# Performance work log

Hardware: AMD Instinct MI355X
Metric: run time of the kernel (lower is better)

The kernel has to match this reference:

```python
import jax, jax.numpy as jnp
import numpy as np

B, L, D = 16, 1024, 256  # batch, c_len == q_len (required by the expand/add in the source), 2*d_model


def mask_logits(x, m):
    # Faithful to the source's (unusual) masking: x*m + x*(1-m)*1e30
    return x * m + x * (1.0 - m) * 1e30


def setup_inputs() -> dict:
    key = jax.random.key(0)
    k = jax.random.split(key, 7)
    c = jax.random.normal(k[0], (B, L, D), dtype=jnp.float32)
    q = jax.random.normal(k[1], (B, L, D), dtype=jnp.float32)
    c_mask = jnp.ones((B, 1, L), dtype=jnp.float32)
    q_mask = jnp.ones((B, 1, L), dtype=jnp.float32)
    # Learned parameters (nn.Parameter zeros in the source; random here so the test is non-degenerate)
    c_weight = jax.random.normal(k[2], (D, 1), dtype=jnp.float32) * 0.05
    q_weight = jax.random.normal(k[3], (D, 1), dtype=jnp.float32) * 0.05
    cq_weight = jax.random.normal(k[4], (1, 1, D), dtype=jnp.float32) * 0.05
    bias = jnp.zeros((1,), dtype=jnp.float32)
    return {"c": c, "q": q, "c_mask": c_mask, "q_mask": q_mask,
            "c_weight": c_weight, "q_weight": q_weight,
            "cq_weight": cq_weight, "bias": bias}


def reference(c, q, c_mask, q_mask, c_weight, q_weight, cq_weight, bias):
    # Dropout treated as identity (inference) for a deterministic reference.
    s0 = jnp.matmul(c, c_weight)                      # [B, L, 1] -> broadcasts over q_len
    s1 = jnp.swapaxes(jnp.matmul(c, q_weight), 1, 2)  # [B, 1, L] (source uses c here, not q)
    s2 = jnp.einsum('bid,bjd->bij', c * cq_weight, q) # [B, L, L]
    S = s0 + s1 + s2 + bias                           # trilinear similarity
    S1 = jax.nn.softmax(mask_logits(S, q_mask), axis=-1)              # [B, Lc, Lq]
    C2Q = jnp.matmul(S1, q)                                           # [B, Lc, D]
    # torch F.softmax with no dim on a 3D tensor defaults to dim=0 (legacy behavior) -> axis=0
    S2 = jax.nn.softmax(mask_logits(jnp.swapaxes(S, 1, 2), c_mask), axis=0)  # [B, Lq, Lc]
    S2 = jnp.matmul(S1, S2)                                           # [B, Lc, Lc]
    Q2C = jnp.matmul(S2, c)                                           # [B, Lc, D]
    # torch.cat default dim=0 -> [4B, Lc, D]
    return jnp.concatenate((c, C2Q, c * C2Q, c * Q2C), axis=0)
```

## Files before the change

### kernel.cpp

```cpp
#include <hip/hip_runtime.h>

typedef __bf16 bf16;
typedef _Float16 f16;
typedef __attribute__((ext_vector_type(8))) __bf16 bf16x8;
typedef __attribute__((ext_vector_type(4))) __bf16 bf16x4;
typedef __attribute__((ext_vector_type(8))) _Float16 f16x8;
typedef __attribute__((ext_vector_type(4))) _Float16 f16x4;
typedef __attribute__((ext_vector_type(4))) float f32x4;

constexpr int Bn = 16, Ln = 1024, Dn = 256;

__device__ __forceinline__ float maskf(float m) { return m + (1.0f - m) * 1e30f; }

__device__ __forceinline__ void gload16(const void* g, void* l) {
  __builtin_amdgcn_global_load_lds((const __attribute__((address_space(1))) void*)g,
                                   (__attribute__((address_space(3))) void*)l, 16, 0, 0);
}

#define VMCNT(N) asm volatile("s_waitcnt vmcnt(" #N ")" ::: "memory")
#define LGKM0 asm volatile("s_waitcnt lgkmcnt(0)" ::: "memory")
#define BARR                                  \
  do {                                        \
    asm volatile("" ::: "memory");            \
    __builtin_amdgcn_s_barrier();             \
    asm volatile("" ::: "memory");            \
  } while (0)

__device__ __forceinline__ void stage512(const bf16* __restrict__ G, int ldg, int k0,
                                         bf16* L, int tid, int wid) {
#pragma unroll
  for (int p = 0; p < 2; ++p) {
    int u = tid + (p << 9);
    int row = u >> 3, s = u & 7;
    int kk = ((s ^ (row & 7)) << 3);
    gload16(G + (size_t)row * ldg + k0 + kk, L + ((p << 9) + (wid << 6)) * 8);
  }
}

__device__ __forceinline__ const bf16* swzp(const bf16* L, int row, int slot) {
  return L + row * 64 + ((slot ^ (row & 7)) << 3);
}

__global__ __launch_bounds__(256) void k_prep2(
    const float* __restrict__ c, const float* __restrict__ q,
    const float* __restrict__ cw, const float* __restrict__ qw,
    const float* __restrict__ cqw, bf16* __restrict__ cm, bf16* __restrict__ qb,
    bf16* __restrict__ cT, bf16* __restrict__ qT,
    float* __restrict__ s0, float* __restrict__ s1, float* __restrict__ outc) {
  __shared__ __align__(16) bf16 tc[32][264];
  __shared__ __align__(16) bf16 tq[32][264];
  int blk = blockIdx.x;
  int b = blk >> 5;
  int l0 = (blk & 31) << 5;
  int t = threadIdx.x;
  int rl = t >> 3;
  int c0 = (t & 7) << 5;
  int grow = b * Ln + l0 + rl;
  size_t base = (size_t)grow * Dn + c0;
  float4 cv[8], qv[8];
#pragma unroll
  for (int k = 0; k < 8; ++k) {
    cv[k] = *(const float4*)&c[base + k * 4];
    qv[k] = *(const float4*)&q[base + k * 4];
  }
  float d0 = 0.f, d1 = 0.f;
#pragma unroll
  for (int k = 0; k < 8; ++k) {
    float4 w = *(const float4*)&cw[c0 + k * 4];
    float4 u = *(const float4*)&qw[c0 + k * 4];
    d0 += cv[k].x * w.x + cv[k].y * w.y + cv[k].z * w.z + cv[k].w * w.w;
    d1 += cv[k].x * u.x + cv[k].y * u.y + cv[k].z * u.z + cv[k].w * u.w;
  }
  d0 += __shfl_xor(d0, 1); d0 += __shfl_xor(d0, 2); d0 += __shfl_xor(d0, 4);
  d1 += __shfl_xor(d1, 1); d1 += __shfl_xor(d1, 2); d1 += __shfl_xor(d1, 4);
  if ((t & 7) == 0) { s0[grow] = d0; s1[grow] = d1; }
#pragma unroll
  for (int k = 0; k < 8; ++k) *(float4*)&outc[base + k * 4] = cv[k];
#pragma unroll
  for (int k2 = 0; k2 < 4; ++k2) {
    float4 m0 = *(const float4*)&cqw[c0 + k2 * 8];
    float4 m1 = *(const float4*)&cqw[c0 + k2 * 8 + 4];
    bf16x8 vm, vq, vc;
#pragma unroll
    for (int e = 0; e < 8; ++e) {
      float cvv = ((const float*)&cv[k2 * 2 + (e >> 2)])[e & 3];
      float qvv = ((const float*)&qv[k2 * 2 + (e >> 2)])[e & 3];
      float mw = (e < 4) ? ((const float*)&m0)[e] : ((const float*)&m1)[e - 4];
      vm[e] = (bf16)(cvv * mw);
      vq[e] = (bf16)qvv;
      vc[e] = (bf16)cvv;
    }
    *(bf16x8*)&cm[base + k2 * 8] = vm;
    *(bf16x8*)&qb[base + k2 * 8] = vq;
    *(bf16x8*)&tc[rl][c0 + k2 * 8] = vc;
    *(bf16x8*)&tq[rl][c0 + k2 * 8] = vq;
  }
  __syncthreads();
  int d = t;
  size_t tb = ((size_t)b * Dn + d) * Ln + l0;
  bf16x8 o[4];
#pragma unroll
  for (int j = 0; j < 4; ++j)
#pragma unroll
    for (int e = 0; e < 8; ++e) o[j][e] = tc[j * 8 + e][d];
#pragma unroll
  for (int j = 0; j < 4; ++j) *(bf16x8*)&cT[tb + j * 8] = o[j];
#pragma unroll
  for (int j = 0; j < 4; ++j)
#pragma unroll
    for (int e = 0; e < 8; ++e) o[j][e] = tq[j * 8 + e][d];
#pragma unroll
  for (int j = 0; j < 4; ++j) *(bf16x8*)&qT[tb + j * 8] = o[j];
}

__global__ __launch_bounds__(512) void g_s(const bf16* __restrict__ Am,
                                           const bf16* __restrict__ Bm,
                                           const float* __restrict__ s0,
                                           const float* __restrict__ s1,
                                           const float* __restrict__ bias,
                                           f16* __restrict__ S) {
  __shared__ __align__(16) bf16 lds[2][2 * 128 * 64];
  int f = blockIdx.x;
  int o = (f & 7) * 128 + (f >> 3);
  int bx = o & 7, by = (o >> 3) & 7, b = o >> 6;
  const bf16* Ab = Am + (size_t)b * Ln * Dn + (size_t)by * 128 * Dn;
  const bf16* Bb = Bm + (size_t)b * Ln * Dn + (size_t)bx * 128 * Dn;
  const int tid = threadIdx.x, wid = tid >> 6, lane = tid & 63;
  const int r = lane & 15, h = lane >> 4, wr = wid >> 2, wc = wid & 3;
  f32x4 acc[4][2];
  f32x4 zero = {0.f, 0.f, 0.f, 0.f};
#pragma unroll
  for (int i = 0; i < 4; ++i)
#pragma unroll
    for (int j = 0; j < 2; ++j) acc[i][j] = zero;

  stage512(Ab, Dn, 0, &lds[0][0], tid, wid);
  stage512(Bb, Dn, 0, &lds[0][8192], tid, wid);
  for (int t = 0; t < 4; ++t) {
    int cur = t & 1;
    if (t < 3) {
      stage512(Ab, Dn, (t + 1) * 64, &lds[cur ^ 1][0], tid, wid);
      stage512(Bb, Dn, (t + 1) * 64, &lds[cur ^ 1][8192], tid, wid);
      VMCNT(4);
    } else {
      VMCNT(0);
    }
    BARR;
    const bf16* lA = &lds[cur][0];
    const bf16* lB = &lds[cur][8192];
#pragma unroll
    for (int kk2 = 0; kk2 < 2; ++kk2) {
      int slot = (kk2 << 2) | h;
      bf16x8 av[4], bv[2];
#pragma unroll
      for (int i = 0; i < 4; ++i)
        av[i] = *(const bf16x8*)swzp(lA, (wr << 6) + (i << 4) + r, slot);
#pragma unroll
      for (int j = 0; j < 2; ++j)
        bv[j] = *(const bf16x8*)swzp(lB, (wc << 5) + (j << 4) + r, slot);
#pragma unroll
      for (int i = 0; i < 4; ++i)
#pragma unroll
        for (int j = 0; j < 2; ++j)
          acc[i][j] = __builtin_amdgcn_mfma_f32_16x16x32_bf16(av[i], bv[j], acc[i][j], 0, 0, 0);
    }
    LGKM0; BARR;
  }
  int grow = by * 128 + wr * 64, gcol = bx * 128 + wc * 32;
  float bvv = bias[0];
  size_t sb = (size_t)b * Ln * Ln;
#pragma unroll
  for (int j = 0; j < 2; ++j) {
    int n = gcol + j * 16 + r;
    float v1 = s1[b * Ln + n];
#pragma unroll
    for (int i = 0; i < 4; ++i) {
      int mb = grow + i * 16 + h * 4;
#pragma unroll
      for (int g = 0; g < 4; ++g) {
        float v0 = s0[b * Ln + mb + g];
        S[sb + (size_t)(mb + g) * Ln + n] = (f16)(acc[i][j][g] + v0 + v1 + bvv);
      }
    }
  }
}

__global__ __launch_bounds__(256) void k_sm(const f16* __restrict__ S,
                                            const float* __restrict__ qmask,
                                            const float* __restrict__ cmask,
                                            bf16* __restrict__ P1,
                                            bf16* __restrict__ P2) {
  __shared__ __align__(16) bf16 tile[16][32][36];
  int blk = blockIdx.x;
  int t = threadIdx.x;
  if (blk < 1024) {
    int i0 = (blk >> 5) << 5, j0 = (blk & 31) << 5;
    int ti = t >> 3, tj4 = (t & 7) << 2;
    int i = i0 + ti;
    const f16* Sp = S + (size_t)i * Ln + j0 + tj4;
    float fm[16];
#pragma unroll
    for (int b = 0; b < 16; ++b) fm[b] = maskf(cmask[b * Ln + i]);
    f16x4 u[16];
#pragma unroll
    for (int b = 0; b < 16; ++b) u[b] = *(const f16x4*)(Sp + (size_t)b * Ln * Ln);
    float m[4] = {-3.4e38f, -3.4e38f, -3.4e38f, -3.4e38f};
#pragma unroll
    for (int b = 0; b < 16; ++b)
#pragma unroll
      for (int g = 0; g < 4; ++g) m[g] = fmaxf(m[g], (float)u[b][g] * fm[b]);
    float e[16][4];
    float s[4] = {0.f, 0.f, 0.f, 0.f};
#pragma unroll
    for (int b = 0; b < 16; ++b)
#pragma unroll
      for (int g = 0; g < 4; ++g) {
        e[b][g] = __expf((float)u[b][g] * fm[b] - m[g]);
        s[g] += e[b][g];
      }
#pragma unroll
    for (int g = 0; g < 4; ++g) s[g] = 1.0f / s[g];
#pragma unroll
    for (int b = 0; b < 16; ++b)
#pragma unroll
      for (int g = 0; g < 4; ++g) tile[b][tj4 + g][ti] = (bf16)(e[b][g] * s[g]);
    __syncthreads();
    int jl = t >> 3, i4 = (t & 7) << 2;
#pragma unroll
    for (int b = 0; b < 16; ++b) {
      *(bf16x4*)&P2[((size_t)b * Ln + j0 + jl) * Ln + i0 + i4] =
          *(const bf16x4*)&tile[b][jl][i4];
    }
  } else {
    int row = (blk - 1024) * 4 + (t >> 6);
    int b = row >> 10;
    int lane = t & 63;
    const f16* Sr = S + (size_t)row * Ln;
    const float* qm = qmask + (size_t)b * Ln;
    float v[16];
    float mx = -3.4e38f;
#pragma unroll
    for (int p = 0; p < 2; ++p) {
      f16x8 x = ((const f16x8*)Sr)[lane + (p << 6)];
      float4 m0 = ((const float4*)qm)[(lane + (p << 6)) * 2];
      float4 m1 = ((const float4*)qm)[(lane + (p << 6)) * 2 + 1];
      float mm[8] = {m0.x, m0.y, m0.z, m0.w, m1.x, m1.y, m1.z, m1.w};
#pragma unroll
      for (int e = 0; e < 8; ++e) {
        float xv = (float)x[e] * maskf(mm[e]);
        v[8 * p + e] = xv;
        mx = fmaxf(mx, xv);
      }
    }
#pragma unroll
    for (int off = 32; off; off >>= 1) mx = fmaxf(mx, __shfl_xor(mx, off));
    float sum = 0.f;
#pragma unroll
    for (int k = 0; k < 16; ++k) {
      v[k] = __expf(v[k] - mx);
      sum += v[k];
    }
#pragma unroll
    for (int off = 32; off; off >>= 1) sum += __shfl_xor(sum, off);
    float inv = 1.0f / sum;
    bf16* Pr = P1 + (size_t)row * Ln;
#pragma unroll
    for (int p = 0; p < 2; ++p) {
      bf16x8 o;
#pragma unroll
      for (int e = 0; e < 8; ++e) o[e] = (bf16)(v[8 * p + e] * inv);
      ((bf16x8*)Pr)[lane + (p << 6)] = o;
    }
  }
}

__global__ __launch_bounds__(512) void g_t(const bf16* __restrict__ cT,
                                           const bf16* __restrict__ P2,
                                           bf16* __restrict__ TT) {
  __shared__ __align__(16) bf16 lds[2][2 * 128 * 64];
  int f = blockIdx.x;
  int o = (f & 7) * 32 + (f >> 3);
  int b = o >> 4, md = (o >> 3) & 1, nb = o & 7;
  const bf16* Ab = cT + (size_t)b * Dn * Ln + (size_t)md * 128 * Ln;
  const bf16* Bb = P2 + (size_t)b * Ln * Ln + (size_t)nb * 128 * Ln;
  const int tid = threadIdx.x, wid = tid >> 6, lane = tid & 63;
  const int r = lane & 15, h = lane >> 4, wr = wid >> 2, wc = wid & 3;
  f32x4 acc[4][2];
  f32x4 zero = {0.f, 0.f, 0.f, 0.f};
#pragma unroll
  for (int i = 0; i < 4; ++i)
#pragma unroll
    for (int j = 0; j < 2; ++j) acc[i][j] = zero;

  stage512(Ab, Ln, 0, &lds[0][0], tid, wid);
  stage512(Bb, Ln, 0, &lds[0][8192], tid, wid);
  for (int t = 0; t < 16; ++t) {
    int cur = t & 1;
    if (t < 15) {
      stage512(Ab, Ln, (t + 1) * 64, &lds[cur ^ 1][0], tid, wid);
      stage512(Bb, Ln, (t + 1) * 64, &lds[cur ^ 1][8192], tid, wid);
      VMCNT(4);
    } else {
      VMCNT(0);
    }
    BARR;
    const bf16* lA = &lds[cur][0];
    const bf16* lB = &lds[cur][8192];
#pragma unroll
    for (int kk2 = 0; kk2 < 2; ++kk2) {
      int slot = (kk2 << 2) | h;
      bf16x8 av[4], bv[2];
#pragma unroll
      for (int i = 0; i < 4; ++i)
        av[i] = *(const bf16x8*)swzp(lA, (wr << 6) + (i << 4) + r, slot);
#pragma unroll
      for (int j = 0; j < 2; ++j)
        bv[j] = *(const bf16x8*)swzp(lB, (wc << 5) + (j << 4) + r, slot);
#pragma unroll
      for (int i = 0; i < 4; ++i)
#pragma unroll
        for (int j = 0; j < 2; ++j)
          acc[i][j] = __builtin_amdgcn_mfma_f32_16x16x32_bf16(av[i], bv[j], acc[i][j], 0, 0, 0);
    }
    LGKM0; BARR;
  }
  size_t ob = (size_t)b * Dn * Ln;
  int dbase = md * 128 + wr * 64, cbase = nb * 128 + wc * 32;
#pragma unroll
  for (int i = 0; i < 4; ++i)
#pragma unroll
    for (int j = 0; j < 2; ++j) {
      int n = cbase + j * 16 + r;
#pragma unroll
      for (int g = 0; g < 4; ++g)
        TT[ob + (size_t)(dbase + i * 16 + h * 4 + g) * Ln + n] = (bf16)acc[i][j][g];
    }
}

__global__ __launch_bounds__(512) void g_cq(const bf16* __restrict__ P1,
                                            const bf16* __restrict__ qT,
                                            const bf16* __restrict__ TT,
                                            const float* __restrict__ c,
                                            float* __restrict__ out) {
  __shared__ __align__(16) bf16 lds[2][3 * 128 * 64];
  int f = blockIdx.x;
  int o = (f & 7) * 32 + (f >> 3);
  int b = o >> 4, by = (o >> 1) & 7, bx = o & 1;
  const bf16* Ab = P1 + (size_t)b * Ln * Ln + (size_t)by * 128 * Ln;
  const bf16* B1 = qT + (size_t)b * Dn * Ln + (size_t)bx * 128 * Ln;
  const bf16* B2 = TT + (size_t)b * Dn * Ln + (size_t)bx * 128 * Ln;
  const int tid = threadIdx.x, wid = tid >> 6, lane = tid & 63;
  const int r = lane & 15, h = lane >> 4, wr = wid >> 2, wc = wid & 3;
  f32x4 acc1[4][2], acc2[4][2];
  f32x4 zero = {0.f, 0.f, 0.f, 0.f};
#pragma unroll
  for (int i = 0; i < 4; ++i)
#pragma unroll
    for (int j = 0; j < 2; ++j) { acc1[i][j] = zero; acc2[i][j] = zero; }

  stage512(Ab, Ln, 0, &lds[0][0], tid, wid);
  stage512(B1, Ln, 0, &lds[0][8192], tid, wid);
  stage512(B2, Ln, 0, &lds[0][16384], tid, wid);
  for (int t = 0; t < 16; ++t) {
    int cur = t & 1;
    if (t < 15) {
      stage512(Ab, Ln, (t + 1) * 64, &lds[cur ^ 1][0], tid, wid);
      stage512(B1, Ln, (t + 1) * 64, &lds[cur ^ 1][8192], tid, wid);
      stage512(B2, Ln, (t + 1) * 64, &lds[cur ^ 1][16384], tid, wid);
      VMCNT(6);
    } else {
      VMCNT(0);
    }
    BARR;
    const bf16* lA = &lds[cur][0];
    const bf16* lB1 = &lds[cur][8192];
    const bf16* lB2 = &lds[cur][16384];
#pragma unroll
    for (int kk2 = 0; kk2 < 2; ++kk2) {
      int slot = (kk2 << 2) | h;
      bf16x8 av[4], bv[2];
#pragma unroll
      for (int i = 0; i < 4; ++i)
        av[i] = *(const bf16x8*)swzp(lA, (wr << 6) + (i << 4) + r, slot);
#pragma unroll
      for (int j = 0; j < 2; ++j)
        bv[j] = *(const bf16x8*)swzp(lB1, (wc << 5) + (j << 4) + r, slot);
#pragma unroll
      for (int i = 0; i < 4; ++i)
#pragma unroll
        for (int j = 0; j < 2; ++j)
          acc1[i][j] = __builtin_amdgcn_mfma_f32_16x16x32_bf16(av[i], bv[j], acc1[i][j], 0, 0, 0);
#pragma unroll
      for (int j = 0; j < 2; ++j)
        bv[j] = *(const bf16x8*)swzp(lB2, (wc << 5) + (j << 4) + r, slot);
#pragma unroll
      for (int i = 0; i < 4; ++i)
#pragma unroll
        for (int j = 0; j < 2; ++j)
          acc2[i][j] = __builtin_amdgcn_mfma_f32_16x16x32_bf16(av[i], bv[j], acc2[i][j], 0, 0, 0);
    }
    LGKM0; BARR;
  }

  int grow = by * 128 + wr * 64, gcol = bx * 128 + wc * 32;
  const float* cb = c + (size_t)b * Ln * Dn;
  float* o1 = out + (size_t)(1 * Bn + b) * Ln * Dn;
  float* o2 = out + (size_t)(2 * Bn + b) * Ln * Dn;
  float* o3 = out + (size_t)(3 * Bn + b) * Ln * Dn;
#pragma unroll
  for (int j = 0; j < 2; ++j) {
    int n = gcol + j * 16 + r;
#pragma unroll
    for (int i = 0; i < 4; ++i) {
      int mb = grow + i * 16 + h * 4;
#pragma unroll
      for (int g = 0; g < 4; ++g) {
        float v1 = acc1[i][j][g];
        float v2 = acc2[i][j][g];
        size_t off = (size_t)(mb + g) * Dn + n;
        float cc = cb[off];
        o1[off] = v1;
        o2[off] = cc * v1;
        o3[off] = cc * v2;
      }
    }
  }
}

extern "C" void kernel_launch(void* const* d_in, const int* in_sizes, int n_in,
                              void* d_out, int out_size, void* d_ws, size_t ws_size,
                              hipStream_t stream) {
  const float* c = (const float*)d_in[0];
  const float* q = (const float*)d_in[1];
  const float* cmask = (const float*)d_in[2];
  const float* qmask = (const float*)d_in[3];
  const float* cw = (const float*)d_in[4];
  const float* qw = (const float*)d_in[5];
  const float* cqw = (const float*)d_in[6];
  const float* bias = (const float*)d_in[7];
  float* out = (float*)d_out;

  char* w = (char*)d_ws;
  f16* S = (f16*)w;       w += (size_t)Bn * Ln * Ln * 2;
  bf16* P1 = (bf16*)w;    w += (size_t)Bn * Ln * Ln * 2;
  bf16* P2 = (bf16*)w;    w += (size_t)Bn * Ln * Ln * 2;
  bf16* cm = (bf16*)w;    w += (size_t)Bn * Ln * Dn * 2;
  bf16* qb = (bf16*)w;    w += (size_t)Bn * Ln * Dn * 2;
  bf16* cT = (bf16*)w;    w += (size_t)Bn * Dn * Ln * 2;
  bf16* qT = (bf16*)w;    w += (size_t)Bn * Dn * Ln * 2;
  bf16* TT = (bf16*)w;    w += (size_t)Bn * Dn * Ln * 2;
  float* s0 = (float*)w;  w += (size_t)Bn * Ln * 4;
  float* s1 = (float*)w;  w += (size_t)Bn * Ln * 4;
  if ((size_t)(w - (char*)d_ws) > ws_size) return;

  k_prep2<<<dim3(Bn * Ln / 32), 256, 0, stream>>>(c, q, cw, qw, cqw, cm, qb, cT, qT, s0, s1, out);
  g_s<<<dim3(1024), 512, 0, stream>>>(cm, qb, s0, s1, bias, S);
  k_sm<<<dim3(1024 + Bn * Ln / 4), 256, 0, stream>>>(S, qmask, cmask, P1, P2);
  g_t<<<dim3(256), 512, 0, stream>>>(cT, P2, TT);
  g_cq<<<dim3(256), 512, 0, stream>>>(P1, qT, TT, c, out);
}
```

Measured before the change: 114.9 us.

## Remap block indices across XCDs, halve softmax LDS tile, raise MFMA wave priority

Block indices in the prep and row-softmax kernels are permuted so that consecutive blocks land on different batches and rows, spreading work across XCD/L2 partitions. The column-softmax transpose tile is halved and written in two passes with an extra barrier, cutting LDS use per block to allow higher occupancy. s_setprio is raised around the MFMA inner loops of the three GEMM kernels so compute waves get issue priority over loading waves. Risks include the extra sync and lost locality from the remapping.

```diff
diff --git a/kernel.cpp b/kernel.cpp
--- a/kernel.cpp
+++ b/kernel.cpp
@@ -49,9 +49,9 @@
     float* __restrict__ s0, float* __restrict__ s1, float* __restrict__ outc) {
   __shared__ __align__(16) bf16 tc[32][264];
   __shared__ __align__(16) bf16 tq[32][264];
-  int blk = blockIdx.x;
-  int b = blk >> 5;
-  int l0 = (blk & 31) << 5;
+  int f = blockIdx.x;
+  int b = ((f & 7) << 1) | ((f >> 8) & 1);
+  int l0 = ((f >> 3) & 31) << 5;
   int t = threadIdx.x;
   int rl = t >> 3;
   int c0 = (t & 7) << 5;
@@ -146,6 +146,7 @@
       VMCNT(0);
     }
     BARR;
+    __builtin_amdgcn_s_setprio(1);
     const bf16* lA = &lds[cur][0];
     const bf16* lB = &lds[cur][8192];
 #pragma unroll
@@ -164,6 +165,7 @@
         for (int j = 0; j < 2; ++j)
           acc[i][j] = __builtin_amdgcn_mfma_f32_16x16x32_bf16(av[i], bv[j], acc[i][j], 0, 0, 0);
     }
+    __builtin_amdgcn_s_setprio(0);
     LGKM0; BARR;
   }
   int grow = by * 128 + wr * 64, gcol = bx * 128 + wc * 32;
@@ -190,7 +192,7 @@
                                             const float* __restrict__ cmask,
                                             bf16* __restrict__ P1,
                                             bf16* __restrict__ P2) {
-  __shared__ __align__(16) bf16 tile[16][32][36];
+  __shared__ __align__(16) bf16 tile[8][32][36];
   int blk = blockIdx.x;
   int t = threadIdx.x;
   if (blk < 1024) {
@@ -220,19 +222,27 @@
       }
 #pragma unroll
     for (int g = 0; g < 4; ++g) s[g] = 1.0f / s[g];
-#pragma unroll
-    for (int b = 0; b < 16; ++b)
-#pragma unroll
-      for (int g = 0; g < 4; ++g) tile[b][tj4 + g][ti] = (bf16)(e[b][g] * s[g]);
-    __syncthreads();
     int jl = t >> 3, i4 = (t & 7) << 2;
 #pragma unroll
-    for (int b = 0; b < 16; ++b) {
-      *(bf16x4*)&P2[((size_t)b * Ln + j0 + jl) * Ln + i0 + i4] =
-          *(const bf16x4*)&tile[b][jl][i4];
+    for (int half = 0; half < 2; ++half) {
+      if (half) __syncthreads();
+#pragma unroll
+      for (int bb = 0; bb < 8; ++bb) {
+        int b = half * 8 + bb;
+#pragma unroll
+        for (int g = 0; g < 4; ++g) tile[bb][tj4 + g][ti] = (bf16)(e[b][g] * s[g]);
+      }
+      __syncthreads();
+#pragma unroll
+      for (int bb = 0; bb < 8; ++bb) {
+        *(bf16x4*)&P2[((size_t)(half * 8 + bb) * Ln + j0 + jl) * Ln + i0 + i4] =
+            *(const bf16x4*)&tile[bb][jl][i4];
+      }
     }
   } else {
-    int row = (blk - 1024) * 4 + (t >> 6);
+    int g = blk - 1024;
+    int rb = ((g & 7) << 9) + (g >> 3);
+    int row = rb * 4 + (t >> 6);
     int b = row >> 10;
     int lane = t & 63;
     const f16* Sr = S + (size_t)row * Ln;
@@ -304,6 +314,7 @@
       VMCNT(0);
     }
     BARR;
+    __builtin_amdgcn_s_setprio(1);
     const bf16* lA = &lds[cur][0];
     const bf16* lB = &lds[cur][8192];
 #pragma unroll
@@ -322,6 +333,7 @@
         for (int j = 0; j < 2; ++j)
           acc[i][j] = __builtin_amdgcn_mfma_f32_16x16x32_bf16(av[i], bv[j], acc[i][j], 0, 0, 0);
     }
+    __builtin_amdgcn_s_setprio(0);
     LGKM0; BARR;
   }
   size_t ob = (size_t)b * Dn * Ln;
@@ -372,6 +384,7 @@
       VMCNT(0);
     }
     BARR;
+    __builtin_amdgcn_s_setprio(1);
     const bf16* lA = &lds[cur][0];
     const bf16* lB1 = &lds[cur][8192];
     const bf16* lB2 = &lds[cur][16384];
@@ -399,6 +412,7 @@
         for (int j = 0; j < 2; ++j)
           acc2[i][j] = __builtin_amdgcn_mfma_f32_16x16x32_bf16(av[i], bv[j], acc2[i][j], 0, 0, 0);
     }
+    __builtin_amdgcn_s_setprio(0);
     LGKM0; BARR;
   }
 
```

Result: slower. 118.6 us (+3.2%).
